# Kernel optimization log

Measured on AMD Instinct MI355X. Metric: run time of the kernel, lower is better.

The kernel has to match this reference:

```python
import jax, jax.numpy as jnp
import numpy as np

NUM_HEADS = 16

def setup_inputs() -> dict:
    key = jax.random.key(0)
    k1, k2, k3 = jax.random.split(key, 3)
    B, N, C = 2, 2048, 1024
    x = jax.random.normal(k1, (B, N, C), dtype=jnp.float32)
    w_qkv = jax.random.normal(k2, (C, 3 * C), dtype=jnp.float32) * (C ** -0.5)
    w_proj = jax.random.normal(k3, (C, C), dtype=jnp.float32) * (C ** -0.5)
    b_proj = jnp.zeros((C,), dtype=jnp.float32)
    return {"x": x, "w_qkv": w_qkv, "w_proj": w_proj, "b_proj": b_proj}

def reference(x, w_qkv, w_proj, b_proj):
    B, N, C = x.shape
    H = NUM_HEADS
    D = C // H
    scale = D ** -0.5
    qkv = x @ w_qkv                               # [B,N,3C]
    qkv = qkv.reshape(B, N, 3, H, D).transpose(2, 0, 3, 1, 4)  # [3,B,H,N,D]
    q, k, v = qkv[0] * scale, qkv[1], qkv[2]
    attn = jnp.einsum('bhnd,bhmd->bhnm', q, k)    # [B,H,N,N]
    attn = jax.nn.softmax(attn, axis=-1)
    out = jnp.einsum('bhnm,bhmd->bhnd', attn, v)  # [B,H,N,D]
    out = out.transpose(0, 2, 1, 3).reshape(B, N, C)
    return out @ w_proj + b_proj
```

## Files before the change

### kernel.cpp

```cpp
#include <hip/hip_runtime.h>

typedef unsigned short ushort_t;
typedef __attribute__((ext_vector_type(8))) short short8;
typedef __attribute__((ext_vector_type(4))) float f32x4;

#define AS1 __attribute__((address_space(1)))
#define AS3 __attribute__((address_space(3)))

#define EXP2F(x) __builtin_amdgcn_exp2f(x)

__device__ __forceinline__ ushort_t f2bf(float f) {
    union { float f; unsigned u; } v; v.f = f;
    unsigned r = v.u + 0x7fffu + ((v.u >> 16) & 1u);
    return (ushort_t)(r >> 16);
}

__device__ __forceinline__ unsigned pack_bf16_pair(float a, float b) {
    unsigned ua = __float_as_uint(a) + 0x8000u;
    unsigned ub = __float_as_uint(b) + 0x8000u;
    return __builtin_amdgcn_perm(ub, ua, 0x07060302u);
}

__device__ __forceinline__ void gl_lds16(const ushort_t* g, ushort_t* lds_base) {
    __builtin_amdgcn_global_load_lds((const AS1 unsigned int*)(size_t)g,
                                     (AS3 unsigned int*)lds_base, 16, 0, 0);
}

#define QSCALE 0.18033688011112042f

__device__ __forceinline__ void transpose_body(
    const float* __restrict__ in, ushort_t* __restrict__ out,
    int K0, int N0, int n, int k0)
{
    ushort_t vals[32];
#pragma unroll
    for (int kk = 0; kk < 32; kk++)
        vals[kk] = f2bf(in[(size_t)(k0 + kk) * N0 + n]);
#pragma unroll
    for (int c = 0; c < 4; c++) {
        short8 v;
#pragma unroll
        for (int e = 0; e < 8; e++) v[e] = (short)vals[c * 8 + e];
        *(short8*)&out[(size_t)n * K0 + k0 + c * 8] = v;
    }
}

__global__ __launch_bounds__(256) void prep_kernel(
    const float* __restrict__ x, const float* __restrict__ wqkv,
    const float* __restrict__ wproj,
    ushort_t* __restrict__ Xb, ushort_t* __restrict__ WqkvT,
    ushort_t* __restrict__ WpT)
{
    const int blk = blockIdx.x, t = threadIdx.x;
    if (blk < 2048) {
        int idx = (blk * 256 + t) * 8;
        float4 a = *(const float4*)&x[idx];
        float4 b = *(const float4*)&x[idx + 4];
        short8 v;
        v[0] = (short)f2bf(a.x); v[1] = (short)f2bf(a.y);
        v[2] = (short)f2bf(a.z); v[3] = (short)f2bf(a.w);
        v[4] = (short)f2bf(b.x); v[5] = (short)f2bf(b.y);
        v[6] = (short)f2bf(b.z); v[7] = (short)f2bf(b.w);
        *(short8*)&Xb[idx] = v;
    } else if (blk < 2048 + 384) {
        int i = blk - 2048;
        transpose_body(wqkv, WqkvT, 1024, 3072, (i % 12) * 256 + t, (i / 12) * 32);
    } else {
        int i = blk - 2432;
        transpose_body(wproj, WpT, 1024, 1024, (i % 4) * 256 + t, (i / 4) * 32);
    }
}

template<int JT>
__device__ __forceinline__ void mfma_gemm_core(
    const ushort_t* __restrict__ A, const ushort_t* __restrict__ Bt,
    int bm, int bn, int w, int lane,
    ushort_t* Atile, ushort_t* Btile, f32x4 acc[4][JT])
{
    const int K = 1024;
    const int wy = w >> 1, wx = w & 1;
    const int lrow8 = lane >> 3;
    const int srcoct = (lane & 7) ^ (lrow8 & 7);
    const int fr = lane & 15, fo = lane >> 4;

    for (int k0 = 0; k0 < K; k0 += 64) {
        __syncthreads();
#pragma unroll
        for (int it = 0; it < 4; it++) {
            int L = w * 4 + it;
            int r = 8 * L + lrow8;
            gl_lds16(A + (size_t)(bm + r) * K + k0 + srcoct * 8, Atile + L * 512);
        }
#pragma unroll
        for (int it = 0; it < JT; it++) {
            int L = w * JT + it;
            int r = 8 * L + lrow8;
            gl_lds16(Bt + (size_t)(bn + r) * K + k0 + srcoct * 8, Btile + L * 512);
        }
        __syncthreads();
#pragma unroll
        for (int s = 0; s < 2; s++) {
            short8 af[4], bf[JT];
#pragma unroll
            for (int i = 0; i < 4; i++) {
                int m = wy * 64 + i * 16 + fr;
                af[i] = *(const short8*)&Atile[m * 64 + (((s * 4 + fo) ^ (m & 7)) * 8)];
            }
#pragma unroll
            for (int j = 0; j < JT; j++) {
                int n = wx * (JT * 16) + j * 16 + fr;
                bf[j] = *(const short8*)&Btile[n * 64 + (((s * 4 + fo) ^ (n & 7)) * 8)];
            }
#pragma unroll
            for (int i = 0; i < 4; i++)
#pragma unroll
                for (int j = 0; j < JT; j++)
                    acc[i][j] = __builtin_amdgcn_mfma_f32_16x16x32_bf16(
                        af[i], bf[j], acc[i][j], 0, 0, 0);
        }
    }
}

__global__ __launch_bounds__(256) void qkv_gemm_kernel(
    const ushort_t* __restrict__ Xb, const ushort_t* __restrict__ WqkvT,
    ushort_t* __restrict__ Qb, ushort_t* __restrict__ Kb, ushort_t* __restrict__ Vtb)
{
    __shared__ __align__(16) ushort_t Atile[128 * 64];
    __shared__ __align__(16) ushort_t Btile[128 * 64];
    const int t = threadIdx.x, w = t >> 6, lane = t & 63;
    const int bm = blockIdx.y * 128, bn = blockIdx.x * 128;

    f32x4 acc[4][4];
#pragma unroll
    for (int i = 0; i < 4; i++)
#pragma unroll
        for (int j = 0; j < 4; j++) acc[i][j] = (f32x4){0.f, 0.f, 0.f, 0.f};

    mfma_gemm_core<4>(Xb, WqkvT, bm, bn, w, lane, Atile, Btile, acc);

    const int wy = w >> 1, wx = w & 1;
    const int colbase = bn + wx * 64 + (lane & 15);
    const int rowbase = bm + wy * 64 + (lane >> 4) * 4;
#pragma unroll
    for (int i = 0; i < 4; i++) {
        int n0 = rowbase + i * 16;
        int b = n0 >> 11, n = n0 & 2047;
#pragma unroll
        for (int j = 0; j < 4; j++) {
            int col = colbase + j * 16;
            f32x4 a = acc[i][j];
            if (col < 1024) {
                int h = col >> 6, d = col & 63;
                size_t base = ((size_t)(b * 16 + h) * 2048 + n) * 64 + d;
#pragma unroll
                for (int r = 0; r < 4; r++)
                    Qb[base + (size_t)r * 64] = f2bf(a[r] * QSCALE);
            } else if (col < 2048) {
                int hc = col & 1023;
                int h = hc >> 6, d = hc & 63;
                size_t base = ((size_t)(b * 16 + h) * 2048 + n) * 64 + d;
#pragma unroll
                for (int r = 0; r < 4; r++)
                    Kb[base + (size_t)r * 64] = f2bf(a[r]);
            } else {
                int hc = col & 1023;
                int h = hc >> 6, d = hc & 63;
                unsigned d0 = pack_bf16_pair(a[0], a[1]);
                unsigned d1 = pack_bf16_pair(a[2], a[3]);
                *(uint2*)&Vtb[((size_t)(b * 16 + h) * 64 + d) * 2048 + n] =
                    make_uint2(d0, d1);
            }
        }
    }
}

__global__ __launch_bounds__(256, 2) void attn_kernel(
    const ushort_t* __restrict__ Q, const ushort_t* __restrict__ K,
    const ushort_t* __restrict__ Vt, ushort_t* __restrict__ O)
{
    __shared__ __align__(16) ushort_t QPs[128 * 64];
    __shared__ __align__(16) ushort_t KV[2][2 * 64 * 64];
    __shared__ float l_lds[128];

    const int lin = blockIdx.x;
    const int xcd = lin & 7, slot = lin >> 3;
    const int bh = xcd * 4 + (slot >> 4);
    const int q0 = (slot & 15) * 128;

    const int t = threadIdx.x, w = t >> 6, lane = t & 63;
    const int lrow8 = lane >> 3;
    const int srcoct = (lane & 7) ^ (lrow8 & 7);
    const int fr = lane & 15, fo = lane >> 4;

    const ushort_t* Qh = Q  + (size_t)bh * 2048 * 64;
    const ushort_t* Kh = K  + (size_t)bh * 2048 * 64;
    const ushort_t* Vh = Vt + (size_t)bh * 64 * 2048;

#pragma unroll
    for (int it = 0; it < 4; it++) {
        int L = w * 4 + it;
        int r = 8 * L + lrow8;
        gl_lds16(Qh + (size_t)(q0 + r) * 64 + srcoct * 8, QPs + L * 512);
    }
#pragma unroll
    for (int it = 0; it < 2; it++) {
        int L = w * 2 + it;
        int r = 16 * w + 8 * it + lrow8;
        gl_lds16(Kh + (size_t)r * 64 + srcoct * 8,   &KV[0][L * 512]);
        gl_lds16(Vh + (size_t)r * 2048 + srcoct * 8, &KV[0][4096 + L * 512]);
    }
    if (t < 128) l_lds[t] = 0.f;
    __syncthreads();

    short8 qf[8][2];
#pragma unroll
    for (int jq = 0; jq < 8; jq++)
#pragma unroll
        for (int s = 0; s < 2; s++) {
            int m = jq * 16 + fr;
            qf[jq][s] = *(const short8*)&QPs[m * 64 + (((s * 4 + fo) ^ (m & 7)) * 8)];
        }
    __syncthreads();

    f32x4 o_acc[2][4];
    float l_part[8];
#pragma unroll
    for (int a = 0; a < 2; a++)
#pragma unroll
        for (int jd = 0; jd < 4; jd++) o_acc[a][jd] = (f32x4){0.f, 0.f, 0.f, 0.f};
#pragma unroll
    for (int j = 0; j < 8; j++) l_part[j] = 0.f;

    int cur = 0;
    for (int kt = 0; kt < 32; kt++) {
        const int u = (kt + 1) & 31;
        const int nxt = cur ^ 1;
#pragma unroll
        for (int it = 0; it < 2; it++) {
            int L = w * 2 + it;
            int r = 16 * w + 8 * it + lrow8;
            gl_lds16(Kh + ((size_t)u * 64 + r) * 64 + srcoct * 8, &KV[nxt][L * 512]);
            gl_lds16(Vh + (size_t)r * 2048 + u * 64 + srcoct * 8, &KV[nxt][4096 + L * 512]);
        }
        const ushort_t* Ks  = KV[cur];
        const ushort_t* Vts = KV[cur] + 4096;

        f32x4 s_acc[8];
#pragma unroll
        for (int j = 0; j < 8; j++) s_acc[j] = (f32x4){0.f, 0.f, 0.f, 0.f};
#pragma unroll
        for (int s = 0; s < 2; s++) {
            int mk = 16 * w + fr;
            short8 kf = *(const short8*)&Ks[mk * 64 + (((s * 4 + fo) ^ (mk & 7)) * 8)];
#pragma unroll
            for (int jq = 0; jq < 8; jq++)
                s_acc[jq] = __builtin_amdgcn_mfma_f32_16x16x32_bf16(
                    kf, qf[jq][s], s_acc[jq], 0, 0, 0);
        }

#pragma unroll
        for (int jq = 0; jq < 8; jq++) {
            float p0 = EXP2F(s_acc[jq][0]);
            float p1 = EXP2F(s_acc[jq][1]);
            float p2 = EXP2F(s_acc[jq][2]);
            float p3 = EXP2F(s_acc[jq][3]);
            l_part[jq] += (p0 + p1) + (p2 + p3);
            unsigned d0 = pack_bf16_pair(p0, p1);
            unsigned d1 = pack_bf16_pair(p2, p3);
            int q   = jq * 16 + fr;
            int oct = 2 * w + (fo >> 1);
            int addr = q * 64 + ((oct ^ (q & 7)) * 8) + (fo & 1) * 4;
            *(uint2*)&QPs[addr] = make_uint2(d0, d1);
        }
        __syncthreads();

#pragma unroll
        for (int s = 0; s < 2; s++) {
            short8 pf[2];
#pragma unroll
            for (int a = 0; a < 2; a++) {
                int mq = 32 * w + 16 * a + fr;
                pf[a] = *(const short8*)&QPs[mq * 64 + (((s * 4 + fo) ^ (mq & 7)) * 8)];
            }
#pragma unroll
            for (int jd = 0; jd < 4; jd++) {
                int nd = jd * 16 + fr;
                short8 vf = *(const short8*)&Vts[nd * 64 + (((s * 4 + fo) ^ (nd & 7)) * 8)];
#pragma unroll
                for (int a = 0; a < 2; a++)
                    o_acc[a][jd] = __builtin_amdgcn_mfma_f32_16x16x32_bf16(
                        pf[a], vf, o_acc[a][jd], 0, 0, 0);
            }
        }
        __syncthreads();
        cur = nxt;
    }

#pragma unroll
    for (int jq = 0; jq < 8; jq++)
        atomicAdd(&l_lds[jq * 16 + fr], l_part[jq]);
    __syncthreads();

    const int b = bh >> 4, h = bh & 15;
#pragma unroll
    for (int a = 0; a < 2; a++)
#pragma unroll
        for (int r = 0; r < 4; r++) {
            int qrow = 32 * w + 16 * a + fo * 4 + r;
            float inv = 1.f / l_lds[qrow];
            int row = b * 2048 + q0 + qrow;
#pragma unroll
            for (int jd = 0; jd < 4; jd++) {
                int col = h * 64 + jd * 16 + fr;
                O[(size_t)row * 1024 + col] = f2bf(o_acc[a][jd][r] * inv);
            }
        }
}

__global__ __launch_bounds__(256) void proj_gemm_kernel(
    const ushort_t* __restrict__ Ao, const ushort_t* __restrict__ WpT,
    const float* __restrict__ bias, float* __restrict__ out)
{
    __shared__ __align__(16) ushort_t Atile[128 * 64];
    __shared__ __align__(16) ushort_t Btile[64 * 64];
    const int t = threadIdx.x, w = t >> 6, lane = t & 63;
    const int bm = blockIdx.y * 128, bn = blockIdx.x * 64;

    f32x4 acc[4][2];
#pragma unroll
    for (int i = 0; i < 4; i++)
#pragma unroll
        for (int j = 0; j < 2; j++) acc[i][j] = (f32x4){0.f, 0.f, 0.f, 0.f};

    mfma_gemm_core<2>(Ao, WpT, bm, bn, w, lane, Atile, Btile, acc);

    const int wy = w >> 1, wx = w & 1;
    const int colbase = bn + wx * 32 + (lane & 15);
    const int rowbase = bm + wy * 64 + (lane >> 4) * 4;
#pragma unroll
    for (int i = 0; i < 4; i++) {
#pragma unroll
        for (int r = 0; r < 4; r++) {
            int row = rowbase + i * 16 + r;
#pragma unroll
            for (int j = 0; j < 2; j++) {
                int col = colbase + j * 16;
                out[(size_t)row * 1024 + col] = acc[i][j][r] + bias[col];
            }
        }
    }
}

extern "C" void kernel_launch(void* const* d_in, const int* in_sizes, int n_in,
                              void* d_out, int out_size, void* d_ws, size_t ws_size,
                              hipStream_t stream) {
    const float* x      = (const float*)d_in[0];
    const float* w_qkv  = (const float*)d_in[1];
    const float* w_proj = (const float*)d_in[2];
    const float* b_proj = (const float*)d_in[3];
    float* out = (float*)d_out;

    char* ws = (char*)d_ws;
    ushort_t* Xb    = (ushort_t*)(ws);
    ushort_t* WqkvT = (ushort_t*)(ws + ((size_t)8  << 20));
    ushort_t* WpT   = (ushort_t*)(ws + ((size_t)14 << 20));
    ushort_t* Qb    = (ushort_t*)(ws + ((size_t)16 << 20));
    ushort_t* Kb    = (ushort_t*)(ws + ((size_t)24 << 20));
    ushort_t* Vtb   = (ushort_t*)(ws + ((size_t)32 << 20));
    ushort_t* Aob   = (ushort_t*)(ws + ((size_t)40 << 20));

    prep_kernel<<<2560, 256, 0, stream>>>(x, w_qkv, w_proj, Xb, WqkvT, WpT);
    qkv_gemm_kernel<<<dim3(24, 32), 256, 0, stream>>>(Xb, WqkvT, Qb, Kb, Vtb);
    attn_kernel<<<dim3(512), 256, 0, stream>>>(Qb, Kb, Vtb, Aob);
    proj_gemm_kernel<<<dim3(16, 32), 256, 0, stream>>>(Aob, WpT, b_proj, out);
}
```

Baseline: 203.5 us.

## Rotate K, V and P LDS buffers to drop the trailing per-iteration barrier

Splits the shared K/V tile into separate buffers: K double-buffered, V triple-buffered, and P double-buffered, with Q staged in the second P buffer. Buffer pointers rotate each iteration, so the end-of-iteration __syncthreads can be removed while the prefetch into the next buffers stays safe. The early barrier after loading Q fragments is removed as well. This cuts one block-wide barrier per key tile, letting warps drift into the next QK^T phase. In exchange, LDS use rises from about 48KB to about 72KB per block, which could limit occupancy.

```diff
diff --git a/kernel.cpp b/kernel.cpp
--- a/kernel.cpp
+++ b/kernel.cpp
@@ -178,8 +178,9 @@
     const ushort_t* __restrict__ Q, const ushort_t* __restrict__ K,
     const ushort_t* __restrict__ Vt, ushort_t* __restrict__ O)
 {
-    __shared__ __align__(16) ushort_t QPs[128 * 64];
-    __shared__ __align__(16) ushort_t KV[2][2 * 64 * 64];
+    __shared__ __align__(16) ushort_t Pbuf[2][128 * 64];
+    __shared__ __align__(16) ushort_t Kbuf[2][64 * 64];
+    __shared__ __align__(16) ushort_t Vbuf[3][64 * 64];
     __shared__ float l_lds[128];
 
     const int lin = blockIdx.x;
@@ -200,14 +201,14 @@
     for (int it = 0; it < 4; it++) {
         int L = w * 4 + it;
         int r = 8 * L + lrow8;
-        gl_lds16(Qh + (size_t)(q0 + r) * 64 + srcoct * 8, QPs + L * 512);
+        gl_lds16(Qh + (size_t)(q0 + r) * 64 + srcoct * 8, &Pbuf[1][L * 512]);
     }
 #pragma unroll
     for (int it = 0; it < 2; it++) {
         int L = w * 2 + it;
         int r = 16 * w + 8 * it + lrow8;
-        gl_lds16(Kh + (size_t)r * 64 + srcoct * 8,   &KV[0][L * 512]);
-        gl_lds16(Vh + (size_t)r * 2048 + srcoct * 8, &KV[0][4096 + L * 512]);
+        gl_lds16(Kh + (size_t)r * 64 + srcoct * 8,   &Kbuf[0][L * 512]);
+        gl_lds16(Vh + (size_t)r * 2048 + srcoct * 8, &Vbuf[0][L * 512]);
     }
     if (t < 128) l_lds[t] = 0.f;
     __syncthreads();
@@ -218,9 +219,8 @@
 #pragma unroll
         for (int s = 0; s < 2; s++) {
             int m = jq * 16 + fr;
-            qf[jq][s] = *(const short8*)&QPs[m * 64 + (((s * 4 + fo) ^ (m & 7)) * 8)];
-        }
-    __syncthreads();
+            qf[jq][s] = *(const short8*)&Pbuf[1][m * 64 + (((s * 4 + fo) ^ (m & 7)) * 8)];
+        }
 
     f32x4 o_acc[2][4];
     float l_part[8];
@@ -231,19 +231,23 @@
 #pragma unroll
     for (int j = 0; j < 8; j++) l_part[j] = 0.f;
 
-    int cur = 0;
+    ushort_t* Vr  = Vbuf[0];
+    ushort_t* Vs1 = Vbuf[1];
+    ushort_t* Vs2 = Vbuf[2];
+    ushort_t* Kr  = Kbuf[0];
+    ushort_t* Kn  = Kbuf[1];
+    ushort_t* Pa  = Pbuf[0];
+    ushort_t* Pb  = Pbuf[1];
+
     for (int kt = 0; kt < 32; kt++) {
         const int u = (kt + 1) & 31;
-        const int nxt = cur ^ 1;
 #pragma unroll
         for (int it = 0; it < 2; it++) {
             int L = w * 2 + it;
             int r = 16 * w + 8 * it + lrow8;
-            gl_lds16(Kh + ((size_t)u * 64 + r) * 64 + srcoct * 8, &KV[nxt][L * 512]);
-            gl_lds16(Vh + (size_t)r * 2048 + u * 64 + srcoct * 8, &KV[nxt][4096 + L * 512]);
-        }
-        const ushort_t* Ks  = KV[cur];
-        const ushort_t* Vts = KV[cur] + 4096;
+            gl_lds16(Kh + ((size_t)u * 64 + r) * 64 + srcoct * 8, Kn  + L * 512);
+            gl_lds16(Vh + (size_t)r * 2048 + u * 64 + srcoct * 8, Vs1 + L * 512);
+        }
 
         f32x4 s_acc[8];
 #pragma unroll
@@ -251,7 +255,7 @@
 #pragma unroll
         for (int s = 0; s < 2; s++) {
             int mk = 16 * w + fr;
-            short8 kf = *(const short8*)&Ks[mk * 64 + (((s * 4 + fo) ^ (mk & 7)) * 8)];
+            short8 kf = *(const short8*)&Kr[mk * 64 + (((s * 4 + fo) ^ (mk & 7)) * 8)];
 #pragma unroll
             for (int jq = 0; jq < 8; jq++)
                 s_acc[jq] = __builtin_amdgcn_mfma_f32_16x16x32_bf16(
@@ -270,7 +274,7 @@
             int q   = jq * 16 + fr;
             int oct = 2 * w + (fo >> 1);
             int addr = q * 64 + ((oct ^ (q & 7)) * 8) + (fo & 1) * 4;
-            *(uint2*)&QPs[addr] = make_uint2(d0, d1);
+            *(uint2*)&Pa[addr] = make_uint2(d0, d1);
         }
         __syncthreads();
 
@@ -280,20 +284,22 @@
 #pragma unroll
             for (int a = 0; a < 2; a++) {
                 int mq = 32 * w + 16 * a + fr;
-                pf[a] = *(const short8*)&QPs[mq * 64 + (((s * 4 + fo) ^ (mq & 7)) * 8)];
+                pf[a] = *(const short8*)&Pa[mq * 64 + (((s * 4 + fo) ^ (mq & 7)) * 8)];
             }
 #pragma unroll
             for (int jd = 0; jd < 4; jd++) {
                 int nd = jd * 16 + fr;
-                short8 vf = *(const short8*)&Vts[nd * 64 + (((s * 4 + fo) ^ (nd & 7)) * 8)];
+                short8 vf = *(const short8*)&Vr[nd * 64 + (((s * 4 + fo) ^ (nd & 7)) * 8)];
 #pragma unroll
                 for (int a = 0; a < 2; a++)
                     o_acc[a][jd] = __builtin_amdgcn_mfma_f32_16x16x32_bf16(
                         pf[a], vf, o_acc[a][jd], 0, 0, 0);
             }
         }
-        __syncthreads();
-        cur = nxt;
+
+        ushort_t* tv = Vr; Vr = Vs1; Vs1 = Vs2; Vs2 = tv;
+        ushort_t* tk = Kr; Kr = Kn; Kn = tk;
+        ushort_t* tp = Pa; Pa = Pb; Pb = tp;
     }
 
 #pragma unroll
```

Result: faster. 199.2 us (-2.1%).
